# Optimization experiments

Hardware: AMD Instinct MI355X
Metric: run time of the kernel (lower is better)

The kernel has to match this reference:

```python
import jax, jax.numpy as jnp
import numpy as np
from jax import lax

B, S, D_IN, D_OUT = 2, 1024, 2048, 2048
H, DK, DV, K = 8, 64, 128, 4
CONV_DIM = H * (3 * DK + DV)  # q,k,f each DK per head; v is DV per head
G = H * DV


def _rsa_scan(q, k, v, f, W):
    # q,k,f: [B,S,H,DK]; v: [B,S,H,DV]; W: [H,DV,DV]
    # matrix-valued per-head state St: [B,H,DK,DV], GRU-style gated update
    qs = jnp.moveaxis(q, 1, 0)
    ks = jnp.moveaxis(k, 1, 0)
    vs = jnp.moveaxis(v, 1, 0)
    fs = jnp.moveaxis(f, 1, 0)
    S0 = jnp.zeros((q.shape[0], H, DK, DV), q.dtype)

    def step(St, xs):
        qt, kt, vt, ft = xs
        g = jax.nn.sigmoid(ft)  # [B,H,DK] forget gate
        cand = jnp.tanh(vt[:, :, None, :] + jnp.einsum('bhkv,hvw->bhkw', St, W))
        St = g[..., None] * St + kt[..., None] * cand  # [B,H,DK,DV]
        yt = jnp.einsum('bhk,bhkv->bhv', qt, St)  # readout [B,H,DV]
        return St, yt

    _, ys = lax.scan(step, S0, (qs, ks, vs, fs))
    return jnp.moveaxis(ys, 0, 1)  # [B,S,H,DV]


def setup_inputs() -> dict:
    key = jax.random.key(0)
    ks = jax.random.split(key, 11)
    std = 0.02
    return {
        'x': jax.random.normal(ks[0], (B, S, D_IN), jnp.float32),
        'w_in': jax.random.normal(ks[1], (CONV_DIM + G, D_IN), jnp.float32) * std,
        'b_in': jax.random.normal(ks[2], (CONV_DIM + G,), jnp.float32) * std,
        'conv_w': jax.random.normal(ks[3], (CONV_DIM, 1, K), jnp.float32) * std,
        'conv_b': jax.random.normal(ks[4], (CONV_DIM,), jnp.float32) * std,
        'D': 1.0 + 0.1 * jax.random.normal(ks[5], (H, DV), jnp.float32),
        'state_weight': jax.random.normal(ks[6], (H, DV, DV), jnp.float32) * std,
        'forget_multiplier': 0.1 * jax.random.normal(ks[7], (H,), jnp.float32),
        'forget_bias': 0.1 * jax.random.normal(ks[8], (H, DK), jnp.float32),
        'g_w': 1.0 + 0.1 * jax.random.normal(ks[9], (G,), jnp.float32),
        'w_out': jax.random.normal(ks[10], (D_OUT, G), jnp.float32) * std,
    }


def reference(x, w_in, b_in, conv_w, conv_b, D, state_weight, forget_multiplier, forget_bias, g_w, w_out):
    h = x @ w_in.T + b_in  # input projection [B,S,CONV_DIM+G]
    conv_in, gate = h[..., :CONV_DIM], h[..., CONV_DIM:]
    # causal depthwise conv1d (left pad K-1) + SiLU activation
    xc = jnp.swapaxes(conv_in, 1, 2)  # [B,C,S]
    yc = lax.conv_general_dilated(xc, conv_w, (1,), [(K - 1, 0)], feature_group_count=CONV_DIM)
    yc = jax.nn.silu(yc + conv_b[None, :, None])
    yc = jnp.swapaxes(yc, 1, 2)  # [B,S,CONV_DIM]
    o = 0
    q = yc[..., o:o + H * DK].reshape(B, S, H, DK); o += H * DK
    k = yc[..., o:o + H * DK].reshape(B, S, H, DK); o += H * DK
    v = yc[..., o:o + H * DV].reshape(B, S, H, DV); o += H * DV
    f = yc[..., o:o + H * DK].reshape(B, S, H, DK)
    # p=2 key normalization over head dim (elementwise_affine=False)
    k = k * lax.rsqrt(jnp.sum(k * k, -1, keepdims=True) + 1e-12)
    f = 2.0 * jax.nn.sigmoid(forget_multiplier)[None, None, :, None] * (f + forget_bias[None, None])
    y = _rsa_scan(q, k, v, f, state_weight)  # [B,S,H,DV]
    y = (y + v * D[None, None]).reshape(B, S, G)
    y = y * jax.nn.silu(gate)
    y = y * lax.rsqrt(jnp.mean(y * y, -1, keepdims=True) + 1e-6) * g_w  # RMSNorm
    return y @ w_out.T
```

## Files before the change

kernel.cpp:

```cpp
#include <hip/hip_runtime.h>

typedef unsigned short u16;
typedef unsigned int u32;
typedef __attribute__((ext_vector_type(8))) short short8;
typedef __attribute__((ext_vector_type(4))) float f32x4;

#define N_B 2
#define N_S 1024
#define N_DIN 2048
#define N_DOUT 2048
#define N_H 8
#define N_DK 64
#define N_DV 128
#define N_CONVD 2560
#define N_G 1024
#define N_NH 3584

#define C_E2 2.88539008f
#define C_E2_INV 0.34657359f

__device__ __forceinline__ u16 f2bf(float f) {
  u32 u = __float_as_uint(f);
  u32 r = (u + 0x7FFFu + ((u >> 16) & 1u)) >> 16;
  return (u16)r;
}
__device__ __forceinline__ float fsigmoid(float x) {
  return __builtin_amdgcn_rcpf(1.f + __builtin_amdgcn_exp2f(-1.44269504f * x));
}
__device__ __forceinline__ u32 pack_bf16_rhu(float a, float b) {
  u32 ua = __float_as_uint(a) + 0x8000u;
  u32 ub = __float_as_uint(b) + 0x8000u;
  return __builtin_amdgcn_perm(ub, ua, 0x07060302u);
}
__device__ __forceinline__ void gload_lds16(const void* g, void* l) {
  __builtin_amdgcn_global_load_lds((const __attribute__((address_space(1))) unsigned int*)g,
                                   (__attribute__((address_space(3))) unsigned int*)l, 16, 0, 0);
}
__device__ __forceinline__ float row16_prefix_sum(float pr) {
  pr += __int_as_float(__builtin_amdgcn_update_dpp(0, __float_as_int(pr), 0x111, 0xF, 0xF, true));
  pr += __int_as_float(__builtin_amdgcn_update_dpp(0, __float_as_int(pr), 0x112, 0xF, 0xF, true));
  pr += __int_as_float(__builtin_amdgcn_update_dpp(0, __float_as_int(pr), 0x114, 0xF, 0xF, true));
  pr += __int_as_float(__builtin_amdgcn_update_dpp(0, __float_as_int(pr), 0x118, 0xF, 0xF, true));
  return pr;
}

__global__ void prep_kernel(const float* __restrict__ x, u16* __restrict__ xb,
                            const float* __restrict__ w_in, u16* __restrict__ wib,
                            const float* __restrict__ wo, u16* __restrict__ wob,
                            const float* __restrict__ sw, u16* __restrict__ wtb) {
  int bid = blockIdx.x;
  if (bid < 11264) {
    const float* src;
    u16* dst;
    int i4;
    if (bid < 4096) { src = x; dst = xb; i4 = (bid * 256 + threadIdx.x) * 4; }
    else { src = w_in; dst = wib; i4 = ((bid - 4096) * 256 + threadIdx.x) * 4; }
    float4 v = *(const float4*)&src[i4];
    dst[i4 + 0] = f2bf(v.x);
    dst[i4 + 1] = f2bf(v.y);
    dst[i4 + 2] = f2bf(v.z);
    dst[i4 + 3] = f2bf(v.w);
  } else if (bid < 13312) {
    int i4 = ((bid - 11264) * 256 + threadIdx.x) * 4;
    float4 v = *(const float4*)&wo[i4];
    wob[i4 + 0] = f2bf(v.x);
    wob[i4 + 1] = f2bf(v.y);
    wob[i4 + 2] = f2bf(v.z);
    wob[i4 + 3] = f2bf(v.w);
  } else {
    int idx = (bid - 13312) * 256 + threadIdx.x;
    int h = idx >> 14;
    int rem = idx & 16383;
    int j = rem >> 7, v = rem & 127;
    wtb[idx] = f2bf(C_E2 * sw[((size_t)h * 128 + v) * 128 + j]);
  }
}

__global__ __launch_bounds__(256, 2) void gemm_bt(const u16* __restrict__ A,
                                                  const u16* __restrict__ B,
                                                  const float* __restrict__ bias,
                                                  float* __restrict__ C, int M, int N, int K) {
  const int tid = threadIdx.x;
  const int lane = tid & 63, w = tid >> 6;
  const int u = lane >> 4, m16 = lane & 15;
  const int wm = w & 1, wn = w >> 1;
  const int m0 = blockIdx.y * 128, n0 = blockIdx.x * 128;

  __shared__ __align__(16) u16 As[128 * 32];
  __shared__ __align__(16) u16 Bs[128 * 32];

  f32x4 acc[4][4];
#pragma unroll
  for (int i = 0; i < 4; ++i)
#pragma unroll
    for (int j = 0; j < 4; ++j)
#pragma unroll
      for (int r = 0; r < 4; ++r) acc[i][j][r] = 0.f;

  for (int kk = 0; kk < K; kk += 32) {
#pragma unroll
    for (int q = 0; q < 2; ++q) {
      int chunk = tid + 256 * q;
      int row = chunk >> 2, col = (chunk & 3) * 8;
      gload_lds16(&A[(size_t)(m0 + row) * K + kk + col], &As[row * 32 + col]);
      gload_lds16(&B[(size_t)(n0 + row) * K + kk + col], &Bs[row * 32 + col]);
    }
    __syncthreads();
    short8 af[4], bfr[4];
#pragma unroll
    for (int i = 0; i < 4; ++i) af[i] = *(const short8*)&As[(64 * wm + 16 * i + m16) * 32 + 8 * u];
#pragma unroll
    for (int i = 0; i < 4; ++i) bfr[i] = *(const short8*)&Bs[(64 * wn + 16 * i + m16) * 32 + 8 * u];
#pragma unroll
    for (int am = 0; am < 4; ++am)
#pragma unroll
      for (int bn = 0; bn < 4; ++bn)
        acc[am][bn] = __builtin_amdgcn_mfma_f32_16x16x32_bf16(af[am], bfr[bn], acc[am][bn], 0, 0, 0);
    __syncthreads();
  }
#pragma unroll
  for (int am = 0; am < 4; ++am)
#pragma unroll
    for (int bn = 0; bn < 4; ++bn) {
      int n = n0 + 64 * wn + 16 * bn + m16;
      float bv = bias ? bias[n] : 0.f;
#pragma unroll
      for (int r = 0; r < 4; ++r) {
        int m = m0 + 64 * wm + 16 * am + 4 * u + r;
        C[(size_t)m * N + n] = acc[am][bn][r] + bv;
      }
    }
}

__global__ void conv_kernel(const float* __restrict__ h, const float* __restrict__ cw,
                            const float* __restrict__ cb, float* __restrict__ SCIN) {
  int gid = blockIdx.x * 256 + threadIdx.x;
  if (gid >= N_B * N_S * N_CONVD) return;
  int c = gid % N_CONVD;
  int bt = gid / N_CONVD;
  int t = bt & 1023, b = bt >> 10;
  float4 wv = *(const float4*)&cw[c * 4];
  const float* wvp = (const float*)&wv;
  float acc = cb[c];
#pragma unroll
  for (int j = 0; j < 4; ++j) {
    int tt = t - 3 + j;
    if (tt >= 0) acc += wvp[j] * h[((size_t)(b * 1024 + tt)) * N_NH + c];
  }
  float yv = acc * fsigmoid(acc);
  if (c >= 1024 && c < 2048) yv *= C_E2;
  int hh, off;
  if (c < 512) { hh = c >> 6; off = c & 63; }
  else if (c < 1024) { int cc = c - 512; hh = cc >> 6; off = 64 + (cc & 63); }
  else if (c < 2048) { int cc = c - 1024; hh = cc >> 7; off = 192 + (cc & 127); }
  else { int cc = c - 2048; hh = cc >> 6; off = 128 + (cc & 63); }
  SCIN[(((size_t)(b * 8 + hh)) * 1024 + t) * 320 + off] = yv;
}

__global__ void prep2_kernel(float* __restrict__ SCIN, const float* __restrict__ fm,
                             const float* __restrict__ fb) {
  int widx = blockIdx.x * 4 + (threadIdx.x >> 6);
  int lane = threadIdx.x & 63;
  int chain = widx >> 10, t = widx & 1023;
  int hh = chain & 7;
  float* base = SCIN + ((size_t)chain * 1024 + t) * 320;
  float kv = base[64 + lane];
  float s = kv * kv;
#pragma unroll
  for (int m = 1; m < 64; m <<= 1) s += __shfl_xor(s, m, 64);
  float inv = __builtin_amdgcn_rsqf(s + 1e-12f);
  base[64 + lane] = kv * inv;
  float fv = base[128 + lane];
  float scale2 = 2.f * fsigmoid(fm[hh]);
  base[128 + lane] = fsigmoid(scale2 * (fv + fb[hh * 64 + lane]));
}

__global__ __launch_bounds__(512, 2) void scan_kernel(const u16* __restrict__ Wtb,
                                                      const float* __restrict__ SCIN,
                                                      float* __restrict__ Ybp) {
  const int tid = threadIdx.x;
  const int lane = tid & 63, wv = tid >> 6;
  const int u = lane >> 4, m16 = lane & 15;
  const int chain = blockIdx.x >> 2;
  const int ig = blockIdx.x & 3;
  const int hh = chain & 7;

  __shared__ __align__(16) u16 Slds[2][16 * 136];

  short8 Wfrag[4];
  {
    const u16* wb = Wtb + ((size_t)hh * 128 + (16 * wv + m16)) * 128 + 8 * u;
#pragma unroll
    for (int kc = 0; kc < 4; ++kc) Wfrag[kc] = *(const short8*)(wb + 32 * kc);
  }

  for (int x = tid; x < 2 * 16 * 136; x += 512) ((u16*)Slds)[x] = 0;

  const float* scin_c = SCIN + (size_t)chain * 1024 * 320;
  float* ybase = Ybp + ((size_t)(chain * 4 + ig)) * 1024 * 128;

  float Sreg[4] = {0.f, 0.f, 0.f, 0.f};
  float pp[4];

  float qv = scin_c[16 * ig + m16];
  float kv = scin_c[64 + 16 * ig + m16];
  float gv = scin_c[128 + 16 * ig + m16];
  f32x4 cv = *(const f32x4*)&scin_c[192 + 16 * wv + 4 * u];

  __syncthreads();

  for (int t = 0; t < 1024; ++t) {
    const u16* Sr = Slds[t & 1];
    u16* Sw = Slds[(t + 1) & 1];

    short8 Bfrag[4];
#pragma unroll
    for (int kc = 0; kc < 4; ++kc)
      Bfrag[kc] = *(const short8*)&Sr[m16 * 136 + 32 * kc + 8 * u];

    const int tn = (t + 1) & 1023;
    const float* pn = scin_c + (size_t)tn * 320;
    float qn = pn[16 * ig + m16];
    float kn = pn[64 + 16 * ig + m16];
    float gn = pn[128 + 16 * ig + m16];
    f32x4 cn = *(const f32x4*)&pn[192 + 16 * wv + 4 * u];

    if (t) {
#pragma unroll
      for (int r = 0; r < 4; ++r) pp[r] = row16_prefix_sum(pp[r]);
      if (m16 == 15) {
        f32x4 yo;
#pragma unroll
        for (int r = 0; r < 4; ++r) yo[r] = pp[r];
        *(f32x4*)(ybase + (size_t)(t - 1) * 128 + 16 * wv + 4 * u) = yo;
      }
    }

    f32x4 a0 = cv, a1 = {0.f, 0.f, 0.f, 0.f};
    a0 = __builtin_amdgcn_mfma_f32_16x16x32_bf16(Wfrag[0], Bfrag[0], a0, 0, 0, 0);
    a1 = __builtin_amdgcn_mfma_f32_16x16x32_bf16(Wfrag[1], Bfrag[1], a1, 0, 0, 0);
    a0 = __builtin_amdgcn_mfma_f32_16x16x32_bf16(Wfrag[2], Bfrag[2], a0, 0, 0, 0);
    a1 = __builtin_amdgcn_mfma_f32_16x16x32_bf16(Wfrag[3], Bfrag[3], a1, 0, 0, 0);

#pragma unroll
    for (int r = 0; r < 4; ++r) {
      float e = __builtin_amdgcn_exp2f(a0[r] + a1[r]);
      float cand = 1.f - 2.f * __builtin_amdgcn_rcpf(e + 1.f);
      Sreg[r] = gv * Sreg[r] + kv * cand;
    }

    uint2 pck;
    pck.x = pack_bf16_rhu(Sreg[0], Sreg[1]);
    pck.y = pack_bf16_rhu(Sreg[2], Sreg[3]);
    *(uint2*)&Sw[m16 * 136 + 16 * wv + 4 * u] = pck;

#pragma unroll
    for (int r = 0; r < 4; ++r) pp[r] = qv * Sreg[r];

    asm volatile("s_waitcnt lgkmcnt(0)\n\ts_barrier" ::: "memory");

    qv = qn; kv = kn; gv = gn; cv = cn;
  }

#pragma unroll
  for (int r = 0; r < 4; ++r) pp[r] = row16_prefix_sum(pp[r]);
  if (m16 == 15) {
    f32x4 yo;
#pragma unroll
    for (int r = 0; r < 4; ++r) yo[r] = pp[r];
    *(f32x4*)(ybase + (size_t)1023 * 128 + 16 * wv + 4 * u) = yo;
  }
}

__global__ __launch_bounds__(256, 2) void post_kernel(const float* __restrict__ Ybp,
                                                      const float* __restrict__ SCIN,
                                                      const float* __restrict__ h,
                                                      const float* __restrict__ Dp,
                                                      const float* __restrict__ gwv,
                                                      u16* __restrict__ Zb) {
  const int bt = blockIdx.x;
  const int b = bt >> 10, t = bt & 1023;
  const int lane = threadIdx.x & 63, wvi = threadIdx.x >> 6;
  float z[4];
  float ss = 0.f;
#pragma unroll
  for (int c = 0; c < 4; ++c) {
    int j = threadIdx.x + 256 * c;
    int head = j >> 7, dv = j & 127;
    int chain = b * 8 + head;
    float y = 0.f;
#pragma unroll
    for (int igx = 0; igx < 4; ++igx)
      y += Ybp[(((size_t)(chain * 4 + igx)) * 1024 + t) * 128 + dv];
    float v = SCIN[((size_t)chain * 1024 + t) * 320 + 192 + dv];
    float gate = h[((size_t)(b * 1024 + t)) * N_NH + 2560 + j];
    float zz = (y + v * (Dp[j] * C_E2_INV)) * (gate * fsigmoid(gate));
    z[c] = zz;
    ss += zz * zz;
  }
#pragma unroll
  for (int m = 1; m < 64; m <<= 1) ss += __shfl_xor(ss, m, 64);
  __shared__ float red[4];
  if (lane == 0) red[wvi] = ss;
  __syncthreads();
  float tot = red[0] + red[1] + red[2] + red[3];
  float scale = __builtin_amdgcn_rsqf(tot * (1.f / 1024.f) + 1e-6f);
#pragma unroll
  for (int c = 0; c < 4; ++c) {
    int j = threadIdx.x + 256 * c;
    Zb[(size_t)(b * 1024 + t) * 1024 + j] = f2bf(z[c] * scale * gwv[j]);
  }
}

extern "C" void kernel_launch(void* const* d_in, const int* in_sizes, int n_in,
                              void* d_out, int out_size, void* d_ws, size_t ws_size,
                              hipStream_t stream) {
  const float* x    = (const float*)d_in[0];
  const float* w_in = (const float*)d_in[1];
  const float* b_in = (const float*)d_in[2];
  const float* cw   = (const float*)d_in[3];
  const float* cb   = (const float*)d_in[4];
  const float* Dp   = (const float*)d_in[5];
  const float* sw   = (const float*)d_in[6];
  const float* fm   = (const float*)d_in[7];
  const float* fb   = (const float*)d_in[8];
  const float* gwv  = (const float*)d_in[9];
  const float* wo   = (const float*)d_in[10];
  float* out = (float*)d_out;

  char* p = (char*)d_ws;
  auto alloc = [&](size_t bytes) {
    char* r = p;
    p += (bytes + 255) & ~(size_t)255;
    return r;
  };
  u16* xb    = (u16*)alloc((size_t)2048 * 2048 * 2);
  u16* wib   = (u16*)alloc((size_t)3584 * 2048 * 2);
  u16* wob   = (u16*)alloc((size_t)2048 * 1024 * 2);
  u16* wtb   = (u16*)alloc((size_t)8 * 128 * 128 * 2);
  float* hbf = (float*)alloc((size_t)2048 * 3584 * 4);
  float* scin= (float*)alloc((size_t)16 * 1024 * 320 * 4);
  float* ybp = (float*)alloc((size_t)64 * 1024 * 128 * 4);
  u16* zb    = (u16*)alloc((size_t)2048 * 1024 * 2);

  prep_kernel<<<13824, 256, 0, stream>>>(x, xb, w_in, wib, wo, wob, sw, wtb);

  gemm_bt<<<dim3(3584 / 128, 2048 / 128), 256, 0, stream>>>(xb, wib, b_in, hbf, 2048, 3584, 2048);

  conv_kernel<<<(N_B * N_S * N_CONVD) / 256, 256, 0, stream>>>(hbf, cw, cb, scin);
  prep2_kernel<<<(16 * 1024) / 4, 256, 0, stream>>>(scin, fm, fb);

  scan_kernel<<<64, 512, 0, stream>>>(wtb, scin, ybp);

  post_kernel<<<2048, 256, 0, stream>>>(ybp, scin, hbf, Dp, gwv, zb);

  gemm_bt<<<dim3(2048 / 128, 2048 / 128), 256, 0, stream>>>(zb, wob, nullptr, out, 2048, 2048, 1024);
}
```

Before: 746.8 us.

## Fuse conv and key/forget prep kernels; restructure scan step readout

Merges the depthwise conv+SiLU kernel and the key-normalisation/forget-gate kernel into one kernel per (b,t) that stages the conv output in shared memory, so the SCIN round trip and a launch are removed. In the scan loop the readout prefix-sum and store for the current step now run in the same iteration rather than being deferred to the next, and the tanh/state update is rewritten as fused multiply-adds. This puts the reduction on the critical path before the barrier, which may lengthen each serial step.

```diff
diff --git a/kernel.cpp b/kernel.cpp
--- a/kernel.cpp
+++ b/kernel.cpp
@@ -35,13 +35,6 @@
 __device__ __forceinline__ void gload_lds16(const void* g, void* l) {
   __builtin_amdgcn_global_load_lds((const __attribute__((address_space(1))) unsigned int*)g,
                                    (__attribute__((address_space(3))) unsigned int*)l, 16, 0, 0);
-}
-__device__ __forceinline__ float row16_prefix_sum(float pr) {
-  pr += __int_as_float(__builtin_amdgcn_update_dpp(0, __float_as_int(pr), 0x111, 0xF, 0xF, true));
-  pr += __int_as_float(__builtin_amdgcn_update_dpp(0, __float_as_int(pr), 0x112, 0xF, 0xF, true));
-  pr += __int_as_float(__builtin_amdgcn_update_dpp(0, __float_as_int(pr), 0x114, 0xF, 0xF, true));
-  pr += __int_as_float(__builtin_amdgcn_update_dpp(0, __float_as_int(pr), 0x118, 0xF, 0xF, true));
-  return pr;
 }
 
 __global__ void prep_kernel(const float* __restrict__ x, u16* __restrict__ xb,
@@ -132,47 +125,55 @@
     }
 }
 
-__global__ void conv_kernel(const float* __restrict__ h, const float* __restrict__ cw,
-                            const float* __restrict__ cb, float* __restrict__ SCIN) {
-  int gid = blockIdx.x * 256 + threadIdx.x;
-  if (gid >= N_B * N_S * N_CONVD) return;
-  int c = gid % N_CONVD;
-  int bt = gid / N_CONVD;
-  int t = bt & 1023, b = bt >> 10;
-  float4 wv = *(const float4*)&cw[c * 4];
-  const float* wvp = (const float*)&wv;
-  float acc = cb[c];
-#pragma unroll
-  for (int j = 0; j < 4; ++j) {
-    int tt = t - 3 + j;
-    if (tt >= 0) acc += wvp[j] * h[((size_t)(b * 1024 + tt)) * N_NH + c];
-  }
-  float yv = acc * fsigmoid(acc);
-  if (c >= 1024 && c < 2048) yv *= C_E2;
-  int hh, off;
-  if (c < 512) { hh = c >> 6; off = c & 63; }
-  else if (c < 1024) { int cc = c - 512; hh = cc >> 6; off = 64 + (cc & 63); }
-  else if (c < 2048) { int cc = c - 1024; hh = cc >> 7; off = 192 + (cc & 127); }
-  else { int cc = c - 2048; hh = cc >> 6; off = 128 + (cc & 63); }
-  SCIN[(((size_t)(b * 8 + hh)) * 1024 + t) * 320 + off] = yv;
-}
-
-__global__ void prep2_kernel(float* __restrict__ SCIN, const float* __restrict__ fm,
-                             const float* __restrict__ fb) {
-  int widx = blockIdx.x * 4 + (threadIdx.x >> 6);
-  int lane = threadIdx.x & 63;
-  int chain = widx >> 10, t = widx & 1023;
-  int hh = chain & 7;
-  float* base = SCIN + ((size_t)chain * 1024 + t) * 320;
-  float kv = base[64 + lane];
-  float s = kv * kv;
-#pragma unroll
-  for (int m = 1; m < 64; m <<= 1) s += __shfl_xor(s, m, 64);
+__global__ __launch_bounds__(256) void convprep_kernel(const float* __restrict__ h,
+                                                       const float* __restrict__ cw,
+                                                       const float* __restrict__ cb,
+                                                       const float* __restrict__ fm,
+                                                       const float* __restrict__ fb,
+                                                       float* __restrict__ SCIN) {
+  const int bt = blockIdx.x;
+  const int t = bt & 1023, b = bt >> 10;
+  const int tid = threadIdx.x;
+  __shared__ float ch[N_CONVD];
+
+#pragma unroll
+  for (int cc = 0; cc < 10; ++cc) {
+    int c = tid + 256 * cc;
+    float4 cwv = *(const float4*)&cw[c * 4];
+    const float* cwp = (const float*)&cwv;
+    float acc = cb[c];
+#pragma unroll
+    for (int j = 0; j < 4; ++j) {
+      int tt = t - 3 + j;
+      if (tt >= 0) acc += cwp[j] * h[((size_t)(b * 1024 + tt)) * N_NH + c];
+    }
+    ch[c] = acc * fsigmoid(acc);
+  }
+  __syncthreads();
+
+  const int hh = tid >> 5, l = tid & 31;
+  float* chainbase = SCIN + ((size_t)(b * 8 + hh) * 1024 + t) * 320;
+
+  float k0 = ch[512 + 64 * hh + l], k1 = ch[512 + 64 * hh + 32 + l];
+  float s = k0 * k0 + k1 * k1;
+#pragma unroll
+  for (int m = 1; m < 32; m <<= 1) s += __shfl_xor(s, m, 64);
   float inv = __builtin_amdgcn_rsqf(s + 1e-12f);
-  base[64 + lane] = kv * inv;
-  float fv = base[128 + lane];
-  float scale2 = 2.f * fsigmoid(fm[hh]);
-  base[128 + lane] = fsigmoid(scale2 * (fv + fb[hh * 64 + lane]));
+  chainbase[64 + l] = k0 * inv;
+  chainbase[64 + 32 + l] = k1 * inv;
+
+  float sc2 = 2.f * fsigmoid(fm[hh]);
+  float f0 = ch[2048 + 64 * hh + l], f1 = ch[2048 + 64 * hh + 32 + l];
+  chainbase[128 + l] = fsigmoid(sc2 * (f0 + fb[hh * 64 + l]));
+  chainbase[128 + 32 + l] = fsigmoid(sc2 * (f1 + fb[hh * 64 + 32 + l]));
+
+  chainbase[l] = ch[64 * hh + l];
+  chainbase[32 + l] = ch[64 * hh + 32 + l];
+
+  chainbase[192 + l] = ch[1024 + 128 * hh + l] * C_E2;
+  chainbase[192 + 32 + l] = ch[1024 + 128 * hh + 32 + l] * C_E2;
+  chainbase[192 + 64 + l] = ch[1024 + 128 * hh + 64 + l] * C_E2;
+  chainbase[192 + 96 + l] = ch[1024 + 128 * hh + 96 + l] * C_E2;
 }
 
 __global__ __launch_bounds__(512, 2) void scan_kernel(const u16* __restrict__ Wtb,
@@ -200,7 +201,6 @@
   float* ybase = Ybp + ((size_t)(chain * 4 + ig)) * 1024 * 128;
 
   float Sreg[4] = {0.f, 0.f, 0.f, 0.f};
-  float pp[4];
 
   float qv = scin_c[16 * ig + m16];
   float kv = scin_c[64 + 16 * ig + m16];
@@ -210,14 +210,6 @@
   __syncthreads();
 
   for (int t = 0; t < 1024; ++t) {
-    const u16* Sr = Slds[t & 1];
-    u16* Sw = Slds[(t + 1) & 1];
-
-    short8 Bfrag[4];
-#pragma unroll
-    for (int kc = 0; kc < 4; ++kc)
-      Bfrag[kc] = *(const short8*)&Sr[m16 * 136 + 32 * kc + 8 * u];
-
     const int tn = (t + 1) & 1023;
     const float* pn = scin_c + (size_t)tn * 320;
     float qn = pn[16 * ig + m16];
@@ -225,16 +217,13 @@
     float gn = pn[128 + 16 * ig + m16];
     f32x4 cn = *(const f32x4*)&pn[192 + 16 * wv + 4 * u];
 
-    if (t) {
-#pragma unroll
-      for (int r = 0; r < 4; ++r) pp[r] = row16_prefix_sum(pp[r]);
-      if (m16 == 15) {
-        f32x4 yo;
-#pragma unroll
-        for (int r = 0; r < 4; ++r) yo[r] = pp[r];
-        *(f32x4*)(ybase + (size_t)(t - 1) * 128 + 16 * wv + 4 * u) = yo;
-      }
-    }
+    const u16* Sr = Slds[t & 1];
+    u16* Sw = Slds[(t + 1) & 1];
+
+    short8 Bfrag[4];
+#pragma unroll
+    for (int kc = 0; kc < 4; ++kc)
+      Bfrag[kc] = *(const short8*)&Sr[m16 * 136 + 32 * kc + 8 * u];
 
     f32x4 a0 = cv, a1 = {0.f, 0.f, 0.f, 0.f};
     a0 = __builtin_amdgcn_mfma_f32_16x16x32_bf16(Wfrag[0], Bfrag[0], a0, 0, 0, 0);
@@ -242,11 +231,15 @@
     a0 = __builtin_amdgcn_mfma_f32_16x16x32_bf16(Wfrag[2], Bfrag[2], a0, 0, 0, 0);
     a1 = __builtin_amdgcn_mfma_f32_16x16x32_bf16(Wfrag[3], Bfrag[3], a1, 0, 0, 0);
 
+    const float k2n = -2.f * kv;
+    float p[4];
 #pragma unroll
     for (int r = 0; r < 4; ++r) {
+      float base = __builtin_fmaf(gv, Sreg[r], kv);
       float e = __builtin_amdgcn_exp2f(a0[r] + a1[r]);
-      float cand = 1.f - 2.f * __builtin_amdgcn_rcpf(e + 1.f);
-      Sreg[r] = gv * Sreg[r] + kv * cand;
+      float d = __builtin_amdgcn_rcpf(e + 1.f);
+      Sreg[r] = __builtin_fmaf(k2n, d, base);
+      p[r] = qv * Sreg[r];
     }
 
     uint2 pck;
@@ -255,20 +248,23 @@
     *(uint2*)&Sw[m16 * 136 + 16 * wv + 4 * u] = pck;
 
 #pragma unroll
-    for (int r = 0; r < 4; ++r) pp[r] = qv * Sreg[r];
+    for (int r = 0; r < 4; ++r) {
+      float pr = p[r];
+      pr += __int_as_float(__builtin_amdgcn_update_dpp(0, __float_as_int(pr), 0x111, 0xF, 0xF, true));
+      pr += __int_as_float(__builtin_amdgcn_update_dpp(0, __float_as_int(pr), 0x112, 0xF, 0xF, true));
+      pr += __int_as_float(__builtin_amdgcn_update_dpp(0, __float_as_int(pr), 0x114, 0xF, 0xF, true));
+      pr += __int_as_float(__builtin_amdgcn_update_dpp(0, __float_as_int(pr), 0x118, 0xF, 0xF, true));
+      p[r] = pr;
+    }
+    if (m16 == 15) {
+      f32x4 yo;
+      yo[0] = p[0]; yo[1] = p[1]; yo[2] = p[2]; yo[3] = p[3];
+      *(f32x4*)(ybase + (size_t)t * 128 + 16 * wv + 4 * u) = yo;
+    }
 
     asm volatile("s_waitcnt lgkmcnt(0)\n\ts_barrier" ::: "memory");
 
     qv = qn; kv = kn; gv = gn; cv = cn;
-  }
-
-#pragma unroll
-  for (int r = 0; r < 4; ++r) pp[r] = row16_prefix_sum(pp[r]);
-  if (m16 == 15) {
-    f32x4 yo;
-#pragma unroll
-    for (int r = 0; r < 4; ++r) yo[r] = pp[r];
-    *(f32x4*)(ybase + (size_t)1023 * 128 + 16 * wv + 4 * u) = yo;
   }
 }
 
@@ -347,8 +343,7 @@
 
   gemm_bt<<<dim3(3584 / 128, 2048 / 128), 256, 0, stream>>>(xb, wib, b_in, hbf, 2048, 3584, 2048);
 
-  conv_kernel<<<(N_B * N_S * N_CONVD) / 256, 256, 0, stream>>>(hbf, cw, cb, scin);
-  prep2_kernel<<<(16 * 1024) / 4, 256, 0, stream>>>(scin, fm, fb);
+  convprep_kernel<<<2048, 256, 0, stream>>>(hbf, cw, cb, fm, fb, scin);
 
   scan_kernel<<<64, 512, 0, stream>>>(wtb, scin, ybp);
 
```

Measured after the change: 641.0 us, median of 2. 1.17x faster.
